# Performance work log

Measured on AMD Instinct MI355X. Metric: run time of the kernel, lower is better.

The kernel has to match this reference:

```python
import jax, jax.numpy as jnp
import numpy as np

# Instant-NGP HashEncoder defaults (torch-ngp) with desired_resolution=2048
L = 16            # num levels
F = 2             # features per level
T = 2 ** 19       # hashmap size per level
BASE = 16         # base resolution
DESIRED = 2048
BOUND = 1.0
PLS = float(np.exp(np.log(DESIRED / BASE) / (L - 1)))
RES = [int(np.ceil(BASE * PLS ** l)) for l in range(L)]  # per-level grid resolution

_OFFS = jnp.array([[i, j, k] for i in range(2) for j in range(2) for k in range(2)], dtype=jnp.uint32)  # [8,3]
_P1 = jnp.uint32(2654435761)
_P2 = jnp.uint32(805459861)


def _level_encode(x01, table, res):
    """x01: [N,3] in [0,1]; table: [T,F]; returns trilinearly-interpolated [N,F]."""
    pos = x01 * res                      # [N,3]
    pf = jnp.floor(pos)
    frac = pos - pf                      # [N,3]
    pi = pf.astype(jnp.uint32)
    corners = pi[:, None, :] + _OFFS[None]  # [N,8,3]
    if (res + 1) ** 3 <= T:
        # dense (collision-free) indexing for coarse levels
        s = jnp.uint32(res + 1)
        idx = corners[..., 0] + s * (corners[..., 1] + s * corners[..., 2])
    else:
        # spatial hash: xor of coordinate * large primes, masked to table size
        idx = (corners[..., 0] ^ (corners[..., 1] * _P1) ^ (corners[..., 2] * _P2)) & jnp.uint32(T - 1)
    # trilinear weights: prod over dims of frac (offset=1) or 1-frac (offset=0)
    w = jnp.prod(jnp.where(_OFFS[None].astype(bool), frac[:, None, :], 1.0 - frac[:, None, :]), axis=-1)  # [N,8]
    return jnp.sum(table[idx] * w[..., None], axis=1)  # [N,F]


def setup_inputs() -> dict:
    key = jax.random.key(0)
    k1, k2, k3, k4 = jax.random.split(key, 4)
    N = 2_097_152
    xyzs = jax.random.uniform(k1, (N, 3), jnp.float32) * 2.0 - 1.0          # in [-bound, bound]
    tables = (jax.random.uniform(k2, (L, T, F), jnp.float32) * 2.0 - 1.0) * 1e-4  # NGP init U(-1e-4,1e-4)
    W1 = jax.random.normal(k3, (L * F, 64), jnp.float32) * (1.0 / np.sqrt(L * F))
    W2 = jax.random.normal(k4, (64, 16), jnp.float32) * (1.0 / np.sqrt(64.0))
    return {"xyzs": xyzs, "tables": tables, "W1": W1, "W2": W2}


def reference(xyzs, tables, W1, W2):
    # normalize to [0,1] using bound (encoder(xyzs, bound))
    x01 = jnp.clip((xyzs + BOUND) / (2.0 * BOUND), 0.0, 1.0)
    enc = jnp.concatenate([_level_encode(x01, tables[l], RES[l]) for l in range(L)], axis=-1)  # [N,32]
    h = jax.nn.relu(enc @ W1)   # [N,64]
    out = h @ W2                # [N,16]
    sigmas = jnp.exp(out[..., 0])   # trunc_exp activation on density channel
    geo_features = out[..., 1:]     # [N,15]
    return sigmas, geo_features
```

## Files before the change

### kernel.cpp

```cpp
#include <hip/hip_runtime.h>
#include <math.h>

#define NLEV 16
#define TSIZE 524288
#define TMASK (TSIZE - 1)
#define P1 2654435761u
#define P2 805459861u
#define NB 32768

struct Params {
    int res[NLEV];
    unsigned ncell[5];
    unsigned doff[5];
};

__device__ __forceinline__ float clamp01f(float v) {
    return fminf(fmaxf(v, 0.0f), 1.0f);
}
__device__ __forceinline__ unsigned f2bf(float f) {
    union { float f; unsigned u; } c; c.f = f;
    return (c.u + 0x7FFFu + ((c.u >> 16) & 1u)) >> 16;
}
__device__ __forceinline__ float bflo(unsigned u) {
    union { unsigned u; float f; } c; c.u = u << 16; return c.f;
}
__device__ __forceinline__ float bfhi(unsigned u) {
    union { unsigned u; float f; } c; c.u = u & 0xFFFF0000u; return c.f;
}
__device__ __forceinline__ unsigned spread5(unsigned v) {
    return (v & 1u) | ((v & 2u) << 2) | ((v & 4u) << 4) |
           ((v & 8u) << 6) | ((v & 16u) << 8);
}
__device__ __forceinline__ unsigned morton_key(float x0, float y0, float z0) {
    unsigned kx = min(31u, (unsigned)(x0 * 32.0f));
    unsigned ky = min(31u, (unsigned)(y0 * 32.0f));
    unsigned kz = min(31u, (unsigned)(z0 * 32.0f));
    return spread5(kx) | (spread5(ky) << 1) | (spread5(kz) << 2);
}

__global__ __launch_bounds__(256) void prep_kernel(
    const float* __restrict__ tables,
    const float* __restrict__ W1,
    const float* __restrict__ W2,
    unsigned* __restrict__ tbl_bf,
    float4* __restrict__ dense_pairs,
    float* __restrict__ W1t, float* __restrict__ W2c,
    Params rp)
{
    const unsigned t = blockIdx.x * 256 + threadIdx.x;
    const unsigned l = t >> 19, c = t & TMASK;
    const float2* t2 = (const float2*)tables;
    if (l >= 5) {
        const float2 v = t2[(size_t)l * TSIZE + c];
        tbl_bf[(size_t)(l - 5) * TSIZE + c] = f2bf(v.x) | (f2bf(v.y) << 16);
    } else if (c < rp.ncell[l]) {
        const float2 a = t2[(size_t)l * TSIZE + c];
        const float2 b = t2[(size_t)l * TSIZE + c + 1];
        dense_pairs[rp.doff[l] + c] = make_float4(a.x, a.y, b.x, b.y);
    }
    if (blockIdx.x == 0) {
        for (int i = threadIdx.x; i < 2048; i += 256)
            W1t[(i & 63) * 32 + (i >> 6)] = W1[i];
        for (int i = threadIdx.x; i < 1024; i += 256)
            W2c[i] = W2[i];
    }
}

__global__ __launch_bounds__(256) void zero_kernel(unsigned* __restrict__ hist) {
    hist[blockIdx.x * 256 + threadIdx.x] = 0u;
}

__global__ __launch_bounds__(256) void hist_kernel(
    const float* __restrict__ xyzs, unsigned* __restrict__ hist)
{
    const int gid = blockIdx.x * 256 + threadIdx.x;
    const float x0 = clamp01f((xyzs[3 * gid + 0] + 1.0f) * 0.5f);
    const float y0 = clamp01f((xyzs[3 * gid + 1] + 1.0f) * 0.5f);
    const float z0 = clamp01f((xyzs[3 * gid + 2] + 1.0f) * 0.5f);
    atomicAdd(&hist[morton_key(x0, y0, z0)], 1u);
}

__global__ __launch_bounds__(1024) void scan_kernel(
    const unsigned* __restrict__ hist, unsigned* __restrict__ work)
{
    __shared__ unsigned part[1024];
    const int tid = threadIdx.x;
    unsigned loc[32], s = 0;
#pragma unroll
    for (int i = 0; i < 32; ++i) { loc[i] = hist[tid * 32 + i]; s += loc[i]; }
    part[tid] = s; __syncthreads();
    for (int st = 1; st < 1024; st <<= 1) {
        unsigned t = (tid >= st) ? part[tid - st] : 0u;
        __syncthreads();
        part[tid] += t;
        __syncthreads();
    }
    unsigned base = (tid == 0) ? 0u : part[tid - 1];
#pragma unroll
    for (int i = 0; i < 32; ++i) { work[tid * 32 + i] = base; base += loc[i]; }
}

__global__ __launch_bounds__(256) void scatter_kernel(
    const float* __restrict__ xyzs, unsigned* __restrict__ work,
    float4* __restrict__ sorted, unsigned* __restrict__ perm)
{
    const int gid = blockIdx.x * 256 + threadIdx.x;
    const float x0 = clamp01f((xyzs[3 * gid + 0] + 1.0f) * 0.5f);
    const float y0 = clamp01f((xyzs[3 * gid + 1] + 1.0f) * 0.5f);
    const float z0 = clamp01f((xyzs[3 * gid + 2] + 1.0f) * 0.5f);
    const unsigned pos = atomicAdd(&work[morton_key(x0, y0, z0)], 1u);
    sorted[pos] = make_float4(x0, y0, z0, 0.0f);
    perm[pos] = (unsigned)gid;
}

__global__ __launch_bounds__(256) void enc_dense_sorted(
    const float4* __restrict__ sorted,
    const float4* __restrict__ dense_pairs,
    unsigned* __restrict__ enc_ws,
    Params rp, int N)
{
    const int gid = blockIdx.x * 256 + threadIdx.x;
    const float4 p = sorted[gid];
    const float x0 = p.x, y0 = p.y, z0 = p.z;

#pragma unroll
    for (int l = 0; l < 5; ++l) {
        const int res = rp.res[l];
        const float rf = (float)res;
        const float px = x0 * rf, py = y0 * rf, pz = z0 * rf;
        const float fx = floorf(px), fy = floorf(py), fz = floorf(pz);
        const float rx = px - fx, ry = py - fy, rz = pz - fz;
        const unsigned ix = (unsigned)fx, iy = (unsigned)fy, iz = (unsigned)fz;

        const unsigned s = (unsigned)(res + 1);
        const unsigned ss = s * s;
        const unsigned a = ix + s * iy + ss * iz;
        const float4* dpt = dense_pairs + rp.doff[l];
        const float4 q00 = dpt[a];
        const float4 q01 = dpt[a + ss];
        const float4 q10 = dpt[a + s];
        const float4 q11 = dpt[a + s + ss];

        const float wx0 = 1.0f - rx, wy0 = 1.0f - ry, wz0 = 1.0f - rz;
        float e0, e1;
        e0  = (wx0 * wy0) * wz0 * q00.x;  e1  = (wx0 * wy0) * wz0 * q00.y;
        e0 += (wx0 * wy0) * rz  * q01.x;  e1 += (wx0 * wy0) * rz  * q01.y;
        e0 += (wx0 * ry ) * wz0 * q10.x;  e1 += (wx0 * ry ) * wz0 * q10.y;
        e0 += (wx0 * ry ) * rz  * q11.x;  e1 += (wx0 * ry ) * rz  * q11.y;
        e0 += (rx  * wy0) * wz0 * q00.z;  e1 += (rx  * wy0) * wz0 * q00.w;
        e0 += (rx  * wy0) * rz  * q01.z;  e1 += (rx  * wy0) * rz  * q01.w;
        e0 += (rx  * ry ) * wz0 * q10.z;  e1 += (rx  * ry ) * wz0 * q10.w;
        e0 += (rx  * ry ) * rz  * q11.z;  e1 += (rx  * ry ) * rz  * q11.w;

        __builtin_nontemporal_store(f2bf(e0) | (f2bf(e1) << 16),
                                    enc_ws + (size_t)l * N + gid);
    }
}

template<int LEVEL>
__global__ __launch_bounds__(256) void enc_hash_sorted(
    const float4* __restrict__ sorted,
    const unsigned* __restrict__ tbl_bf,
    unsigned* __restrict__ enc_ws,
    int res, int N)
{
    const int g0 = blockIdx.x * 512 + threadIdx.x;
    const unsigned* tl = tbl_bf + (size_t)(LEVEL - 5) * TSIZE;
    const float rf = (float)res;

    int gid[2] = { g0, g0 + 256 };
    unsigned v[2][8];
    float rx[2], ry[2], rz[2];

#pragma unroll
    for (int p = 0; p < 2; ++p) {
        const float4 pt = sorted[gid[p]];
        const float px = pt.x * rf, py = pt.y * rf, pz = pt.z * rf;
        const float fx = floorf(px), fy = floorf(py), fz = floorf(pz);
        rx[p] = px - fx; ry[p] = py - fy; rz[p] = pz - fz;
        const unsigned ix = (unsigned)fx, iy = (unsigned)fy, iz = (unsigned)fz;
        const unsigned ax0 = ix,        ax1 = ix + 1u;
        const unsigned by0 = iy * P1,   by1 = (iy + 1u) * P1;
        const unsigned cz0 = iz * P2,   cz1 = (iz + 1u) * P2;
        unsigned idx[8];
        idx[0] = (ax0 ^ by0 ^ cz0) & TMASK;
        idx[1] = (ax0 ^ by0 ^ cz1) & TMASK;
        idx[2] = (ax0 ^ by1 ^ cz0) & TMASK;
        idx[3] = (ax0 ^ by1 ^ cz1) & TMASK;
        idx[4] = (ax1 ^ by0 ^ cz0) & TMASK;
        idx[5] = (ax1 ^ by0 ^ cz1) & TMASK;
        idx[6] = (ax1 ^ by1 ^ cz0) & TMASK;
        idx[7] = (ax1 ^ by1 ^ cz1) & TMASK;
#pragma unroll
        for (int c = 0; c < 8; ++c) v[p][c] = tl[idx[c]];
    }

#pragma unroll
    for (int p = 0; p < 2; ++p) {
        const float wx0 = 1.0f - rx[p], wy0 = 1.0f - ry[p], wz0 = 1.0f - rz[p];
        float e0 = 0.0f, e1 = 0.0f;
#pragma unroll
        for (int c = 0; c < 8; ++c) {
            const float wx = (c & 4) ? rx[p] : wx0;
            const float wy = (c & 2) ? ry[p] : wy0;
            const float wz = (c & 1) ? rz[p] : wz0;
            const float w = (wx * wy) * wz;
            e0 += w * bflo(v[p][c]);
            e1 += w * bfhi(v[p][c]);
        }
        __builtin_nontemporal_store(f2bf(e0) | (f2bf(e1) << 16),
                                    enc_ws + (size_t)LEVEL * N + gid[p]);
    }
}

__global__ __launch_bounds__(256) void mlp_scatter_kernel(
    const unsigned* __restrict__ enc_ws,
    const unsigned* __restrict__ perm,
    const float* __restrict__ W1t,
    const float* __restrict__ W2c,
    float* __restrict__ out_sigma,
    float* __restrict__ out_geo,
    int N)
{
    __shared__ float sW1t[64 * 32];
    __shared__ float sW2[64 * 16];

    const int tid = threadIdx.x;
    for (int i = tid; i < 2048; i += 256) sW1t[i] = W1t[i];
    for (int i = tid; i < 1024; i += 256) sW2[i] = W2c[i];
    __syncthreads();

    const int pt0 = blockIdx.x * 512 + tid;
    const int pt1 = pt0 + 256;

    float ea[32], eb[32];
#pragma unroll
    for (int l = 0; l < NLEV; ++l) {
        const unsigned u0 = __builtin_nontemporal_load(enc_ws + (size_t)l * N + pt0);
        const unsigned u1 = __builtin_nontemporal_load(enc_ws + (size_t)l * N + pt1);
        ea[2 * l] = bflo(u0); ea[2 * l + 1] = bfhi(u0);
        eb[2 * l] = bflo(u1); eb[2 * l + 1] = bfhi(u1);
    }

    float oa[16], ob[16];
#pragma unroll
    for (int q = 0; q < 16; ++q) { oa[q] = 0.0f; ob[q] = 0.0f; }

    for (int j = 0; j < 64; ++j) {
        const float4* wr = (const float4*)&sW1t[j * 32];
        float h0 = 0.0f, h1 = 0.0f;
#pragma unroll
        for (int k = 0; k < 8; ++k) {
            const float4 w = wr[k];
            h0 += ea[4 * k + 0] * w.x; h1 += eb[4 * k + 0] * w.x;
            h0 += ea[4 * k + 1] * w.y; h1 += eb[4 * k + 1] * w.y;
            h0 += ea[4 * k + 2] * w.z; h1 += eb[4 * k + 2] * w.z;
            h0 += ea[4 * k + 3] * w.w; h1 += eb[4 * k + 3] * w.w;
        }
        h0 = fmaxf(h0, 0.0f); h1 = fmaxf(h1, 0.0f);
        const float4* w2 = (const float4*)&sW2[j * 16];
#pragma unroll
        for (int q = 0; q < 4; ++q) {
            const float4 w = w2[q];
            oa[4 * q + 0] += h0 * w.x; ob[4 * q + 0] += h1 * w.x;
            oa[4 * q + 1] += h0 * w.y; ob[4 * q + 1] += h1 * w.y;
            oa[4 * q + 2] += h0 * w.z; ob[4 * q + 2] += h1 * w.z;
            oa[4 * q + 3] += h0 * w.w; ob[4 * q + 3] += h1 * w.w;
        }
    }

    const unsigned o0 = perm[pt0];
    const unsigned o1 = perm[pt1];
    out_sigma[o0] = expf(oa[0]);
    out_sigma[o1] = expf(ob[0]);
#pragma unroll
    for (int q = 1; q < 16; ++q)
        out_geo[(size_t)o0 * 15 + (q - 1)] = oa[q];
#pragma unroll
    for (int q = 1; q < 16; ++q)
        out_geo[(size_t)o1 * 15 + (q - 1)] = ob[q];
}

__global__ __launch_bounds__(256) void hashgrid_fused_kernel(
    const float* __restrict__ xyzs,
    const float* __restrict__ tables,
    const float* __restrict__ W1,
    const float* __restrict__ W2,
    float* __restrict__ out_sigma,
    float* __restrict__ out_geo,
    Params rp, int ndense)
{
    __shared__ float sW1t[64 * 32];
    __shared__ float sW2[64 * 16];
    __shared__ float sGeo[256 * 15];

    const int tid = threadIdx.x;
    for (int i = tid; i < 2048; i += 256) {
        int k = i >> 6, j = i & 63;
        sW1t[j * 32 + k] = W1[i];
    }
    for (int i = tid; i < 1024; i += 256) sW2[i] = W2[i];
    __syncthreads();

    const int gid = blockIdx.x * 256 + tid;
    const float x0 = clamp01f((xyzs[3 * gid + 0] + 1.0f) * 0.5f);
    const float y0 = clamp01f((xyzs[3 * gid + 1] + 1.0f) * 0.5f);
    const float z0 = clamp01f((xyzs[3 * gid + 2] + 1.0f) * 0.5f);

    float enc[32];
    const float2* tb = (const float2*)tables;

#pragma unroll
    for (int l = 0; l < NLEV; ++l) {
        const int res = rp.res[l];
        const float rf = (float)res;
        const float px = x0 * rf, py = y0 * rf, pz = z0 * rf;
        const float fx = floorf(px), fy = floorf(py), fz = floorf(pz);
        const float rx = px - fx, ry = py - fy, rz = pz - fz;
        const unsigned ix = (unsigned)fx, iy = (unsigned)fy, iz = (unsigned)fz;

        unsigned idx[8];
        if (l < ndense) {
            const unsigned s = (unsigned)(res + 1);
            const unsigned ss = s * s;
            const unsigned base = ix + s * (iy + s * iz);
            idx[0] = base;          idx[1] = base + ss;
            idx[2] = base + s;      idx[3] = base + s + ss;
            idx[4] = base + 1u;     idx[5] = base + 1u + ss;
            idx[6] = base + 1u + s; idx[7] = base + 1u + s + ss;
        } else {
            const unsigned ax0 = ix,        ax1 = ix + 1u;
            const unsigned by0 = iy * P1,   by1 = (iy + 1u) * P1;
            const unsigned cz0 = iz * P2,   cz1 = (iz + 1u) * P2;
            idx[0] = (ax0 ^ by0 ^ cz0) & TMASK;
            idx[1] = (ax0 ^ by0 ^ cz1) & TMASK;
            idx[2] = (ax0 ^ by1 ^ cz0) & TMASK;
            idx[3] = (ax0 ^ by1 ^ cz1) & TMASK;
            idx[4] = (ax1 ^ by0 ^ cz0) & TMASK;
            idx[5] = (ax1 ^ by0 ^ cz1) & TMASK;
            idx[6] = (ax1 ^ by1 ^ cz0) & TMASK;
            idx[7] = (ax1 ^ by1 ^ cz1) & TMASK;
        }

        const float2* tl = tb + (size_t)l * TSIZE;
        float2 v[8];
#pragma unroll
        for (int c = 0; c < 8; ++c) v[c] = tl[idx[c]];

        const float wx0 = 1.0f - rx, wy0 = 1.0f - ry, wz0 = 1.0f - rz;
        float e0 = 0.0f, e1 = 0.0f;
#pragma unroll
        for (int c = 0; c < 8; ++c) {
            const float wx = (c & 4) ? rx : wx0;
            const float wy = (c & 2) ? ry : wy0;
            const float wz = (c & 1) ? rz : wz0;
            const float w = (wx * wy) * wz;
            e0 += w * v[c].x;
            e1 += w * v[c].y;
        }
        enc[2 * l]     = e0;
        enc[2 * l + 1] = e1;
    }

    float outv[16];
#pragma unroll
    for (int q = 0; q < 16; ++q) outv[q] = 0.0f;

    for (int j = 0; j < 64; ++j) {
        const float4* wrow = (const float4*)&sW1t[j * 32];
        float hj = 0.0f;
#pragma unroll
        for (int kk = 0; kk < 8; ++kk) {
            const float4 wv = wrow[kk];
            hj += enc[4 * kk + 0] * wv.x;
            hj += enc[4 * kk + 1] * wv.y;
            hj += enc[4 * kk + 2] * wv.z;
            hj += enc[4 * kk + 3] * wv.w;
        }
        hj = fmaxf(hj, 0.0f);
        const float4* w2row = (const float4*)&sW2[j * 16];
#pragma unroll
        for (int qq = 0; qq < 4; ++qq) {
            const float4 w2v = w2row[qq];
            outv[4 * qq + 0] += hj * w2v.x;
            outv[4 * qq + 1] += hj * w2v.y;
            outv[4 * qq + 2] += hj * w2v.z;
            outv[4 * qq + 3] += hj * w2v.w;
        }
    }

    out_sigma[gid] = expf(outv[0]);

    const int wave = tid >> 6;
    const int lane = tid & 63;
    float* gs = &sGeo[wave * 960];
#pragma unroll
    for (int q = 1; q < 16; ++q) gs[lane * 15 + (q - 1)] = outv[q];
    __syncthreads();
    const size_t wbase = (size_t)(blockIdx.x * 256 + wave * 64) * 15;
#pragma unroll
    for (int j = 0; j < 15; ++j)
        out_geo[wbase + (size_t)(j * 64 + lane)] = gs[j * 64 + lane];
}

extern "C" void kernel_launch(void* const* d_in, const int* in_sizes, int n_in,
                              void* d_out, int out_size, void* d_ws, size_t ws_size,
                              hipStream_t stream) {
    const float* xyzs   = (const float*)d_in[0];
    const float* tables = (const float*)d_in[1];
    const float* W1     = (const float*)d_in[2];
    const float* W2     = (const float*)d_in[3];
    float* out = (float*)d_out;

    const int N = in_sizes[0] / 3;

    Params rp;
    int ndense = 0;
    const double PLS = exp(log(2048.0 / 16.0) / 15.0);
    bool pattern_ok = true;
    for (int l = 0; l < NLEV; ++l) {
        const double r = ceil(16.0 * pow(PLS, (double)l));
        rp.res[l] = (int)r;
        const long long s = (long long)r + 1;
        const bool dense = (s * s * s <= (long long)TSIZE);
        if (dense) ndense = l + 1;
        if (dense != (l < 5)) pattern_ok = false;
    }
    unsigned doff = 0;
    if (pattern_ok) {
        for (int l = 0; l < 5; ++l) {
            const unsigned s = (unsigned)rp.res[l] + 1;
            rp.ncell[l] = s * s * s;
            rp.doff[l] = doff;
            doff += rp.ncell[l];
        }
    }

    float* out_sigma = out;
    float* out_geo   = out + N;

    const size_t dpB  = (size_t)doff * 16;
    const size_t srtB = (size_t)N * 16;
    const size_t encB = (size_t)NLEV * N * 4;
    const size_t tblB = (size_t)11 * TSIZE * 4;
    const size_t prmB = (size_t)N * 4;
    const size_t hstB = (size_t)NB * 4;
    const size_t need = dpB + srtB + encB + tblB + prmB + 2 * hstB + 3072 * 4;

    if (pattern_ok && ws_size >= need) {
        char* w = (char*)d_ws;
        float4*   dense_pairs = (float4*)w;              w += dpB;
        float4*   sorted      = (float4*)w;              w += srtB;
        unsigned* enc_ws      = (unsigned*)w;            w += encB;
        unsigned* tbl_bf      = (unsigned*)w;            w += tblB;
        unsigned* perm        = (unsigned*)w;            w += prmB;
        unsigned* hist        = (unsigned*)w;            w += hstB;
        unsigned* work        = (unsigned*)w;            w += hstB;
        float*    W1t         = (float*)w;               w += 2048 * 4;
        float*    W2c         = (float*)w;

        prep_kernel<<<dim3(NLEV * TSIZE / 256), dim3(256), 0, stream>>>(
            tables, W1, W2, tbl_bf, dense_pairs, W1t, W2c, rp);

        zero_kernel<<<dim3(NB / 256), dim3(256), 0, stream>>>(hist);
        hist_kernel<<<dim3(N / 256), dim3(256), 0, stream>>>(xyzs, hist);
        scan_kernel<<<dim3(1), dim3(1024), 0, stream>>>(hist, work);
        scatter_kernel<<<dim3(N / 256), dim3(256), 0, stream>>>(
            xyzs, work, sorted, perm);

        enc_dense_sorted<<<dim3(N / 256), dim3(256), 0, stream>>>(
            sorted, dense_pairs, enc_ws, rp, N);

        const dim3 g2(N / 512), blk(256);
        enc_hash_sorted< 5><<<g2, blk, 0, stream>>>(sorted, tbl_bf, enc_ws, rp.res[ 5], N);
        enc_hash_sorted< 6><<<g2, blk, 0, stream>>>(sorted, tbl_bf, enc_ws, rp.res[ 6], N);
        enc_hash_sorted< 7><<<g2, blk, 0, stream>>>(sorted, tbl_bf, enc_ws, rp.res[ 7], N);
        enc_hash_sorted< 8><<<g2, blk, 0, stream>>>(sorted, tbl_bf, enc_ws, rp.res[ 8], N);
        enc_hash_sorted< 9><<<g2, blk, 0, stream>>>(sorted, tbl_bf, enc_ws, rp.res[ 9], N);
        enc_hash_sorted<10><<<g2, blk, 0, stream>>>(sorted, tbl_bf, enc_ws, rp.res[10], N);
        enc_hash_sorted<11><<<g2, blk, 0, stream>>>(sorted, tbl_bf, enc_ws, rp.res[11], N);
        enc_hash_sorted<12><<<g2, blk, 0, stream>>>(sorted, tbl_bf, enc_ws, rp.res[12], N);
        enc_hash_sorted<13><<<g2, blk, 0, stream>>>(sorted, tbl_bf, enc_ws, rp.res[13], N);
        enc_hash_sorted<14><<<g2, blk, 0, stream>>>(sorted, tbl_bf, enc_ws, rp.res[14], N);
        enc_hash_sorted<15><<<g2, blk, 0, stream>>>(sorted, tbl_bf, enc_ws, rp.res[15], N);

        mlp_scatter_kernel<<<dim3(N / 512), blk, 0, stream>>>(
            enc_ws, perm, W1t, W2c, out_sigma, out_geo, N);
    } else {
        hashgrid_fused_kernel<<<dim3(N / 256), dim3(256), 0, stream>>>(
            xyzs, tables, W1, W2, out_sigma, out_geo, rp, ndense);
    }
}
```

Baseline: 1.233 ms.

## Run MLP on bf16 MFMA with split-precision weights and widen hash gather batching

Replaces the scalar FP32 MLP with a matrix-core version using 16x16x32 bf16 MFMA. Weights and hidden activations are split into hi/lo bf16 parts so the products keep near-FP32 accuracy, and the hidden layer is staged through swizzled shared memory. The hash-level encoder now processes four points per thread instead of two for more outstanding gathers, and uses nontemporal loads on the finer levels. This is meant to cut the ALU cost of the MLP and raise memory-level parallelism in the gathers, at the cost of more registers and a small precision risk.

```diff
diff --git a/kernel.cpp b/kernel.cpp
--- a/kernel.cpp
+++ b/kernel.cpp
@@ -14,6 +14,12 @@
     unsigned doff[5];
 };
 
+typedef short short8 __attribute__((ext_vector_type(8)));
+typedef float f32x4 __attribute__((ext_vector_type(4)));
+
+union U4S8 { uint4 u; short8 s; };
+__device__ __forceinline__ short8 as_s8(uint4 u) { U4S8 x; x.u = u; return x.s; }
+
 __device__ __forceinline__ float clamp01f(float v) {
     return fminf(fmaxf(v, 0.0f), 1.0f);
 }
@@ -44,7 +50,7 @@
     const float* __restrict__ W2,
     unsigned* __restrict__ tbl_bf,
     float4* __restrict__ dense_pairs,
-    float* __restrict__ W1t, float* __restrict__ W2c,
+    unsigned* __restrict__ wf,
     Params rp)
 {
     const unsigned t = blockIdx.x * 256 + threadIdx.x;
@@ -59,10 +65,22 @@
         dense_pairs[rp.doff[l] + c] = make_float4(a.x, a.y, b.x, b.y);
     }
     if (blockIdx.x == 0) {
-        for (int i = threadIdx.x; i < 2048; i += 256)
-            W1t[(i & 63) * 32 + (i >> 6)] = W1[i];
-        for (int i = threadIdx.x; i < 1024; i += 256)
-            W2c[i] = W2[i];
+        for (int idx = threadIdx.x; idx < 1024; idx += 256) {
+            const int jt = idx >> 8, rem = idx & 255, ln = rem >> 2, m = rem & 3;
+            const int k0 = 8 * (ln >> 4) + 2 * m, j = 16 * jt + (ln & 15);
+            const float f0 = W1[k0 * 64 + j], f1 = W1[(k0 + 1) * 64 + j];
+            const unsigned h0 = f2bf(f0), h1 = f2bf(f1);
+            wf[idx] = h0 | (h1 << 16);
+            wf[1024 + idx] = f2bf(f0 - bflo(h0)) | (f2bf(f1 - bflo(h1)) << 16);
+        }
+        for (int idx = threadIdx.x; idx < 512; idx += 256) {
+            const int s = idx >> 8, rem = idx & 255, ln = rem >> 2, m = rem & 3;
+            const int k0 = 32 * s + 8 * (ln >> 4) + 2 * m, q = ln & 15;
+            const float f0 = W2[k0 * 16 + q], f1 = W2[(k0 + 1) * 16 + q];
+            const unsigned h0 = f2bf(f0), h1 = f2bf(f1);
+            wf[2048 + idx] = h0 | (h1 << 16);
+            wf[2560 + idx] = f2bf(f0 - bflo(h0)) | (f2bf(f1 - bflo(h1)) << 16);
+        }
     }
 }
 
@@ -157,24 +175,23 @@
     }
 }
 
-template<int LEVEL>
+template<int LEVEL, int NT>
 __global__ __launch_bounds__(256) void enc_hash_sorted(
     const float4* __restrict__ sorted,
     const unsigned* __restrict__ tbl_bf,
     unsigned* __restrict__ enc_ws,
     int res, int N)
 {
-    const int g0 = blockIdx.x * 512 + threadIdx.x;
+    const int g0 = blockIdx.x * 1024 + threadIdx.x;
     const unsigned* tl = tbl_bf + (size_t)(LEVEL - 5) * TSIZE;
     const float rf = (float)res;
 
-    int gid[2] = { g0, g0 + 256 };
-    unsigned v[2][8];
-    float rx[2], ry[2], rz[2];
-
-#pragma unroll
-    for (int p = 0; p < 2; ++p) {
-        const float4 pt = sorted[gid[p]];
+    unsigned v[4][8];
+    float rx[4], ry[4], rz[4];
+
+#pragma unroll
+    for (int p = 0; p < 4; ++p) {
+        const float4 pt = sorted[g0 + 256 * p];
         const float px = pt.x * rf, py = pt.y * rf, pz = pt.z * rf;
         const float fx = floorf(px), fy = floorf(py), fz = floorf(pz);
         rx[p] = px - fx; ry[p] = py - fy; rz[p] = pz - fz;
@@ -192,11 +209,12 @@
         idx[6] = (ax1 ^ by1 ^ cz0) & TMASK;
         idx[7] = (ax1 ^ by1 ^ cz1) & TMASK;
 #pragma unroll
-        for (int c = 0; c < 8; ++c) v[p][c] = tl[idx[c]];
-    }
-
-#pragma unroll
-    for (int p = 0; p < 2; ++p) {
+        for (int c = 0; c < 8; ++c)
+            v[p][c] = NT ? __builtin_nontemporal_load(tl + idx[c]) : tl[idx[c]];
+    }
+
+#pragma unroll
+    for (int p = 0; p < 4; ++p) {
         const float wx0 = 1.0f - rx[p], wy0 = 1.0f - ry[p], wz0 = 1.0f - rz[p];
         float e0 = 0.0f, e1 = 0.0f;
 #pragma unroll
@@ -209,76 +227,93 @@
             e1 += w * bfhi(v[p][c]);
         }
         __builtin_nontemporal_store(f2bf(e0) | (f2bf(e1) << 16),
-                                    enc_ws + (size_t)LEVEL * N + gid[p]);
-    }
-}
-
-__global__ __launch_bounds__(256) void mlp_scatter_kernel(
+                                    enc_ws + (size_t)LEVEL * N + g0 + 256 * p);
+    }
+}
+
+__global__ __launch_bounds__(256) void mlp_mfma_kernel(
     const unsigned* __restrict__ enc_ws,
     const unsigned* __restrict__ perm,
-    const float* __restrict__ W1t,
-    const float* __restrict__ W2c,
+    const unsigned* __restrict__ wf,
     float* __restrict__ out_sigma,
     float* __restrict__ out_geo,
     int N)
 {
-    __shared__ float sW1t[64 * 32];
-    __shared__ float sW2[64 * 16];
-
-    const int tid = threadIdx.x;
-    for (int i = tid; i < 2048; i += 256) sW1t[i] = W1t[i];
-    for (int i = tid; i < 1024; i += 256) sW2[i] = W2c[i];
-    __syncthreads();
-
-    const int pt0 = blockIdx.x * 512 + tid;
-    const int pt1 = pt0 + 256;
-
-    float ea[32], eb[32];
-#pragma unroll
-    for (int l = 0; l < NLEV; ++l) {
-        const unsigned u0 = __builtin_nontemporal_load(enc_ws + (size_t)l * N + pt0);
-        const unsigned u1 = __builtin_nontemporal_load(enc_ws + (size_t)l * N + pt1);
-        ea[2 * l] = bflo(u0); ea[2 * l + 1] = bfhi(u0);
-        eb[2 * l] = bflo(u1); eb[2 * l + 1] = bfhi(u1);
-    }
-
-    float oa[16], ob[16];
-#pragma unroll
-    for (int q = 0; q < 16; ++q) { oa[q] = 0.0f; ob[q] = 0.0f; }
-
-    for (int j = 0; j < 64; ++j) {
-        const float4* wr = (const float4*)&sW1t[j * 32];
-        float h0 = 0.0f, h1 = 0.0f;
-#pragma unroll
-        for (int k = 0; k < 8; ++k) {
-            const float4 w = wr[k];
-            h0 += ea[4 * k + 0] * w.x; h1 += eb[4 * k + 0] * w.x;
-            h0 += ea[4 * k + 1] * w.y; h1 += eb[4 * k + 1] * w.y;
-            h0 += ea[4 * k + 2] * w.z; h1 += eb[4 * k + 2] * w.z;
-            h0 += ea[4 * k + 3] * w.w; h1 += eb[4 * k + 3] * w.w;
-        }
-        h0 = fmaxf(h0, 0.0f); h1 = fmaxf(h1, 0.0f);
-        const float4* w2 = (const float4*)&sW2[j * 16];
-#pragma unroll
-        for (int q = 0; q < 4; ++q) {
-            const float4 w = w2[q];
-            oa[4 * q + 0] += h0 * w.x; ob[4 * q + 0] += h1 * w.x;
-            oa[4 * q + 1] += h0 * w.y; ob[4 * q + 1] += h1 * w.y;
-            oa[4 * q + 2] += h0 * w.z; ob[4 * q + 2] += h1 * w.z;
-            oa[4 * q + 3] += h0 * w.w; ob[4 * q + 3] += h1 * w.w;
-        }
-    }
-
-    const unsigned o0 = perm[pt0];
-    const unsigned o1 = perm[pt1];
-    out_sigma[o0] = expf(oa[0]);
-    out_sigma[o1] = expf(ob[0]);
-#pragma unroll
-    for (int q = 1; q < 16; ++q)
-        out_geo[(size_t)o0 * 15 + (q - 1)] = oa[q];
-#pragma unroll
-    for (int q = 1; q < 16; ++q)
-        out_geo[(size_t)o1 * 15 + (q - 1)] = ob[q];
+    __shared__ short sH[4][4096];
+
+    const int tid  = threadIdx.x;
+    const int wid  = tid >> 6;
+    const int lane = tid & 63;
+    const int l15  = lane & 15;
+    const int b    = lane >> 4;
+    const int wbase = blockIdx.x * 256 + wid * 64;
+    short* sHw = &sH[wid][0];
+
+    uint4 w1h[4], w1l[4], w2h[2], w2l[2];
+#pragma unroll
+    for (int t = 0; t < 4; ++t) {
+        w1h[t] = *(const uint4*)&wf[t * 256 + lane * 4];
+        w1l[t] = *(const uint4*)&wf[1024 + t * 256 + lane * 4];
+    }
+#pragma unroll
+    for (int s = 0; s < 2; ++s) {
+        w2h[s] = *(const uint4*)&wf[2048 + s * 256 + lane * 4];
+        w2l[s] = *(const uint4*)&wf[2560 + s * 256 + lane * 4];
+    }
+
+    uint4 af[4];
+#pragma unroll
+    for (int pt = 0; pt < 4; ++pt) {
+        const int p = wbase + 16 * pt + l15;
+        af[pt].x = __builtin_nontemporal_load(enc_ws + (size_t)(4 * b + 0) * N + p);
+        af[pt].y = __builtin_nontemporal_load(enc_ws + (size_t)(4 * b + 1) * N + p);
+        af[pt].z = __builtin_nontemporal_load(enc_ws + (size_t)(4 * b + 2) * N + p);
+        af[pt].w = __builtin_nontemporal_load(enc_ws + (size_t)(4 * b + 3) * N + p);
+    }
+
+#pragma unroll
+    for (int pt = 0; pt < 4; ++pt) {
+        const short8 a = as_s8(af[pt]);
+        f32x4 c[4];
+#pragma unroll
+        for (int jt = 0; jt < 4; ++jt) {
+            f32x4 z = {0.f, 0.f, 0.f, 0.f};
+            z = __builtin_amdgcn_mfma_f32_16x16x32_bf16(a, as_s8(w1l[jt]), z, 0, 0, 0);
+            z = __builtin_amdgcn_mfma_f32_16x16x32_bf16(a, as_s8(w1h[jt]), z, 0, 0, 0);
+            c[jt] = z;
+        }
+#pragma unroll
+        for (int jt = 0; jt < 4; ++jt) {
+#pragma unroll
+            for (int r = 0; r < 4; ++r) {
+                const int rowpt = 4 * b + r;
+                const int chunk = 2 * jt + (l15 >> 3);
+                const int swz = chunk ^ (rowpt & 7);
+                const int off = rowpt * 64 + swz * 8 + (l15 & 7);
+                const float h = fmaxf(c[jt][r], 0.0f);
+                const unsigned hh = f2bf(h);
+                sHw[off] = (short)hh;
+                sHw[2048 + off] = (short)f2bf(h - bflo(hh));
+            }
+        }
+        f32x4 c2 = {0.f, 0.f, 0.f, 0.f};
+#pragma unroll
+        for (int s = 0; s < 2; ++s) {
+            const int off = (l15 * 8 + ((4 * s + b) ^ (l15 & 7))) * 8;
+            const short8 ahi = as_s8(*(const uint4*)&sHw[off]);
+            const short8 alo = as_s8(*(const uint4*)&sHw[2048 + off]);
+            c2 = __builtin_amdgcn_mfma_f32_16x16x32_bf16(ahi, as_s8(w2l[s]), c2, 0, 0, 0);
+            c2 = __builtin_amdgcn_mfma_f32_16x16x32_bf16(alo, as_s8(w2h[s]), c2, 0, 0, 0);
+            c2 = __builtin_amdgcn_mfma_f32_16x16x32_bf16(ahi, as_s8(w2h[s]), c2, 0, 0, 0);
+        }
+#pragma unroll
+        for (int r = 0; r < 4; ++r) {
+            const unsigned o = perm[wbase + 16 * pt + 4 * b + r];
+            const float v = c2[r];
+            if (l15 == 0) out_sigma[o] = expf(v);
+            else          out_geo[(size_t)o * 15 + (l15 - 1)] = v;
+        }
+    }
 }
 
 __global__ __launch_bounds__(256) void hashgrid_fused_kernel(
@@ -445,7 +480,8 @@
     const size_t tblB = (size_t)11 * TSIZE * 4;
     const size_t prmB = (size_t)N * 4;
     const size_t hstB = (size_t)NB * 4;
-    const size_t need = dpB + srtB + encB + tblB + prmB + 2 * hstB + 3072 * 4;
+    const size_t wfB  = 3072 * 4;
+    const size_t need = dpB + srtB + encB + tblB + prmB + 2 * hstB + wfB;
 
     if (pattern_ok && ws_size >= need) {
         char* w = (char*)d_ws;
@@ -456,11 +492,10 @@
         unsigned* perm        = (unsigned*)w;            w += prmB;
         unsigned* hist        = (unsigned*)w;            w += hstB;
         unsigned* work        = (unsigned*)w;            w += hstB;
-        float*    W1t         = (float*)w;               w += 2048 * 4;
-        float*    W2c         = (float*)w;
+        unsigned* wf          = (unsigned*)w;
 
         prep_kernel<<<dim3(NLEV * TSIZE / 256), dim3(256), 0, stream>>>(
-            tables, W1, W2, tbl_bf, dense_pairs, W1t, W2c, rp);
+            tables, W1, W2, tbl_bf, dense_pairs, wf, rp);
 
         zero_kernel<<<dim3(NB / 256), dim3(256), 0, stream>>>(hist);
         hist_kernel<<<dim3(N / 256), dim3(256), 0, stream>>>(xyzs, hist);
@@ -471,21 +506,21 @@
         enc_dense_sorted<<<dim3(N / 256), dim3(256), 0, stream>>>(
             sorted, dense_pairs, enc_ws, rp, N);
 
-        const dim3 g2(N / 512), blk(256);
-        enc_hash_sorted< 5><<<g2, blk, 0, stream>>>(sorted, tbl_bf, enc_ws, rp.res[ 5], N);
-        enc_hash_sorted< 6><<<g2, blk, 0, stream>>>(sorted, tbl_bf, enc_ws, rp.res[ 6], N);
-        enc_hash_sorted< 7><<<g2, blk, 0, stream>>>(sorted, tbl_bf, enc_ws, rp.res[ 7], N);
-        enc_hash_sorted< 8><<<g2, blk, 0, stream>>>(sorted, tbl_bf, enc_ws, rp.res[ 8], N);
-        enc_hash_sorted< 9><<<g2, blk, 0, stream>>>(sorted, tbl_bf, enc_ws, rp.res[ 9], N);
-        enc_hash_sorted<10><<<g2, blk, 0, stream>>>(sorted, tbl_bf, enc_ws, rp.res[10], N);
-        enc_hash_sorted<11><<<g2, blk, 0, stream>>>(sorted, tbl_bf, enc_ws, rp.res[11], N);
-        enc_hash_sorted<12><<<g2, blk, 0, stream>>>(sorted, tbl_bf, enc_ws, rp.res[12], N);
-        enc_hash_sorted<13><<<g2, blk, 0, stream>>>(sorted, tbl_bf, enc_ws, rp.res[13], N);
-        enc_hash_sorted<14><<<g2, blk, 0, stream>>>(sorted, tbl_bf, enc_ws, rp.res[14], N);
-        enc_hash_sorted<15><<<g2, blk, 0, stream>>>(sorted, tbl_bf, enc_ws, rp.res[15], N);
-
-        mlp_scatter_kernel<<<dim3(N / 512), blk, 0, stream>>>(
-            enc_ws, perm, W1t, W2c, out_sigma, out_geo, N);
+        const dim3 g4(N / 1024), blk(256);
+        enc_hash_sorted< 5,0><<<g4, blk, 0, stream>>>(sorted, tbl_bf, enc_ws, rp.res[ 5], N);
+        enc_hash_sorted< 6,0><<<g4, blk, 0, stream>>>(sorted, tbl_bf, enc_ws, rp.res[ 6], N);
+        enc_hash_sorted< 7,0><<<g4, blk, 0, stream>>>(sorted, tbl_bf, enc_ws, rp.res[ 7], N);
+        enc_hash_sorted< 8,0><<<g4, blk, 0, stream>>>(sorted, tbl_bf, enc_ws, rp.res[ 8], N);
+        enc_hash_sorted< 9,1><<<g4, blk, 0, stream>>>(sorted, tbl_bf, enc_ws, rp.res[ 9], N);
+        enc_hash_sorted<10,1><<<g4, blk, 0, stream>>>(sorted, tbl_bf, enc_ws, rp.res[10], N);
+        enc_hash_sorted<11,1><<<g4, blk, 0, stream>>>(sorted, tbl_bf, enc_ws, rp.res[11], N);
+        enc_hash_sorted<12,1><<<g4, blk, 0, stream>>>(sorted, tbl_bf, enc_ws, rp.res[12], N);
+        enc_hash_sorted<13,1><<<g4, blk, 0, stream>>>(sorted, tbl_bf, enc_ws, rp.res[13], N);
+        enc_hash_sorted<14,1><<<g4, blk, 0, stream>>>(sorted, tbl_bf, enc_ws, rp.res[14], N);
+        enc_hash_sorted<15,1><<<g4, blk, 0, stream>>>(sorted, tbl_bf, enc_ws, rp.res[15], N);
+
+        mlp_mfma_kernel<<<dim3(N / 256), blk, 0, stream>>>(
+            enc_ws, perm, wf, out_sigma, out_geo, N);
     } else {
         hashgrid_fused_kernel<<<dim3(N / 256), dim3(256), 0, stream>>>(
             xyzs, tables, W1, W2, out_sigma, out_geo, rp, ndense);
```

New measurement: 1.896 ms. 1.54x slower.
